# Optimization experiments

Hardware: AMD Instinct MI355X
Metric: run time of the kernel (lower is better)

## Reference

```python
import jax, jax.numpy as jnp
import numpy as np

EPS = 1e-6

def rmsnorm(x, w):
    v = jnp.mean(jnp.square(x), axis=-1, keepdims=True)
    return x * jax.lax.rsqrt(v + EPS) * w

def setup_inputs() -> dict:
    key = jax.random.key(0)
    ks = jax.random.split(key, 12)
    H, Di, L = 2048, 4096, 1024   # hidden, mamba inner (expand*H), seq tokens
    DT, N, K = 128, 16, 4         # dt_rank, d_state, d_conv
    F = 8192                      # MLP intermediate
    s = lambda k, shp, sc: jax.random.normal(k, shp, jnp.float32) * sc
    return dict(
        hidden_states=s(ks[0], (L, H), 1.0),
        in_ln_w=jnp.ones((H,), jnp.float32),
        pre_ff_ln_w=jnp.ones((H,), jnp.float32),
        in_proj_w=s(ks[1], (2 * Di, H), 0.02),
        conv_w=s(ks[2], (Di, K), 0.1),
        conv_b=s(ks[3], (Di,), 0.1),
        x_proj_w=s(ks[4], (DT + 2 * N, Di), 0.02),
        dt_ln_w=jnp.ones((DT,), jnp.float32),
        b_ln_w=jnp.ones((N,), jnp.float32),
        c_ln_w=jnp.ones((N,), jnp.float32),
        dt_proj_w=s(ks[5], (Di, DT), 0.02),
        dt_proj_b=s(ks[6], (Di,), 0.1),
        A=-jnp.exp(jax.random.uniform(ks[7], (Di, N), jnp.float32, -4.0, 0.0)),
        D=jnp.ones((Di,), jnp.float32),
        out_proj_w=s(ks[8], (H, Di), 0.02),
        gate_up_w=s(ks[9], (2 * F, H), 0.02),
        down_w=s(ks[10], (H, F), 0.02),
    )

def reference(hidden_states, in_ln_w, pre_ff_ln_w, in_proj_w, conv_w, conv_b,
              x_proj_w, dt_ln_w, b_ln_w, c_ln_w, dt_proj_w, dt_proj_b,
              A, D, out_proj_w, gate_up_w, down_w):
    residual = hidden_states
    x = rmsnorm(hidden_states, in_ln_w)
    # --- Mamba mixer (prefill / selective_scan path) ---
    proj = x @ in_proj_w.T                          # [L, 2*Di]
    Di = in_proj_w.shape[0] // 2
    h, gate = proj[:, :Di], proj[:, Di:]
    # causal depthwise conv1d, kernel K, left pad K-1, then silu
    K = conv_w.shape[1]
    L = h.shape[0]
    hp = jnp.pad(h, ((K - 1, 0), (0, 0)))           # [L+K-1, Di]
    idx = jnp.arange(L)[:, None] + jnp.arange(K)[None, :]
    h = jnp.einsum('lkd,dk->ld', hp[idx], conv_w) + conv_b
    h = jax.nn.silu(h)
    # ssm parameters
    ssm = h @ x_proj_w.T                            # [L, DT+2N]
    DTr = dt_ln_w.shape[0]
    N = b_ln_w.shape[0]
    dt = rmsnorm(ssm[:, :DTr], dt_ln_w)
    B = rmsnorm(ssm[:, DTr:DTr + N], b_ln_w)
    C = rmsnorm(ssm[:, DTr + N:], c_ln_w)
    delta = jax.nn.softplus(dt @ dt_proj_w.T + dt_proj_b)   # [L, Di]
    # selective scan (discretize then linear recurrence over L)
    dA = jnp.exp(delta[:, :, None] * A[None, :, :])         # [L, Di, N]
    dBu = delta[:, :, None] * B[:, None, :] * h[:, :, None] # [L, Di, N]
    def step(s, inp):
        da, dbu = inp
        s = da * s + dbu
        return s, s
    s0 = jnp.zeros((Di, N), jnp.float32)
    _, states = jax.lax.scan(step, s0, (dA, dBu))           # [L, Di, N]
    y = jnp.einsum('ldn,ln->ld', states, C) + h * D
    y = y * jax.nn.silu(gate)
    mixer_out = y @ out_proj_w.T                    # [L, H]
    # --- residual + pre-FF norm + gated MLP ---
    residual = residual + mixer_out
    x = rmsnorm(residual, pre_ff_ln_w)
    gu = x @ gate_up_w.T                            # [L, 2F]
    F = down_w.shape[1]
    x = jax.nn.silu(gu[:, :F]) * gu[:, F:]
    ff = x @ down_w.T
    return residual + ff
```

## Files before the change

kernel.cpp:

```cpp
#include <hip/hip_runtime.h>
#include <math.h>

typedef unsigned short u16;
typedef __bf16 bf16x8 __attribute__((ext_vector_type(8)));
typedef short s16x8 __attribute__((ext_vector_type(8)));
typedef short s16x4 __attribute__((ext_vector_type(4)));
typedef float f32x4 __attribute__((ext_vector_type(4)));

__device__ __forceinline__ u16 f2bf(float f) {
  union { float f; unsigned u; } v; v.f = f;
  unsigned u = v.u;
  unsigned r = u + 0x7fffu + ((u >> 16) & 1u);
  return (u16)(r >> 16);
}
__device__ __forceinline__ float bf2f(u16 h) {
  union { unsigned u; float f; } v; v.u = ((unsigned)h) << 16;
  return v.f;
}
__device__ __forceinline__ float fast_softplus(float x) {
  return (x > 20.f) ? x : __logf(1.f + __expf(x));
}
__device__ __forceinline__ float fast_sig(float x) {
  return __builtin_amdgcn_rcpf(1.f + __expf(-x));
}

__device__ __forceinline__ void gld_lds16(const u16* g, u16* l) {
  __builtin_amdgcn_global_load_lds(
      (const __attribute__((address_space(1))) unsigned int*)g,
      (__attribute__((address_space(3))) unsigned int*)l, 16, 0, 0);
}

__global__ __launch_bounds__(256)
void f32_to_bf16_k(const float* __restrict__ src, u16* __restrict__ dst,
                   int n, int n_valid) {
  int i = (blockIdx.x * 256 + threadIdx.x) * 4;
  if (i >= n) return;
  s16x4 o;
  if (i + 3 < n_valid) {
    float4 v = *(const float4*)(src + i);
    o[0] = (short)f2bf(v.x); o[1] = (short)f2bf(v.y);
    o[2] = (short)f2bf(v.z); o[3] = (short)f2bf(v.w);
  } else {
    o[0] = 0; o[1] = 0; o[2] = 0; o[3] = 0;
  }
  *(s16x4*)(dst + i) = o;
}

template <int BN, int MODE>
__global__ __launch_bounds__(256)
void gemm2(const u16* __restrict__ A, const u16* __restrict__ B,
           float* __restrict__ C, u16* __restrict__ Cb,
           const u16* __restrict__ aux, int M, int Nc, int K) {
  constexpr int NJ = BN / 32;
  constexpr int BISS = BN / 32;
  __shared__ __align__(16) u16 As[64 * 64];
  __shared__ __align__(16) u16 Bs[BN * 64];
  const int tid = threadIdx.x;
  const int tm0 = blockIdx.y * 64;
  const int tn0 = blockIdx.x * BN;
  const int wave = tid >> 6;
  const int lane = tid & 63;
  const int wm = (wave >> 1) * 32;
  const int wn = (wave & 1) * (BN / 2);
  const int frow = lane & 15;
  const int fc = lane >> 4;
  const int rmask = frow & 7;

  const int r0 = tid >> 3;
  const int csw = (((tid & 7) ^ (r0 & 7)) << 3);
  const u16* gA = A + (size_t)(tm0 + r0) * K + csw;
  const u16* gB = B + (size_t)(tn0 + r0) * K + csw;
  u16* lA = &As[tid * 8];
  u16* lB = &Bs[tid * 8];

  f32x4 acc[2][NJ];
  f32x4 zero = {0.f, 0.f, 0.f, 0.f};
#pragma unroll
  for (int i = 0; i < 2; ++i)
#pragma unroll
    for (int j = 0; j < NJ; ++j) acc[i][j] = zero;

  for (int kt = 0; kt < K; kt += 64) {
    __syncthreads();
    gld_lds16(gA, lA);
    gld_lds16(gA + (size_t)32 * K, lA + 2048);
#pragma unroll
    for (int b = 0; b < BISS; ++b)
      gld_lds16(gB + (size_t)32 * b * K, lB + b * 2048);
    gA += 64; gB += 64;
    __syncthreads();
#pragma unroll
    for (int s = 0; s < 2; ++s) {
      bf16x8 af[2], bfr[NJ];
#pragma unroll
      for (int i = 0; i < 2; ++i) {
        int addr = (wm + i * 16 + frow) * 64 + (((s * 4 + fc) ^ rmask) << 3);
        af[i] = __builtin_bit_cast(bf16x8, *(const s16x8*)&As[addr]);
      }
#pragma unroll
      for (int j = 0; j < NJ; ++j) {
        int addr = (wn + j * 16 + frow) * 64 + (((s * 4 + fc) ^ rmask) << 3);
        bfr[j] = __builtin_bit_cast(bf16x8, *(const s16x8*)&Bs[addr]);
      }
#pragma unroll
      for (int i = 0; i < 2; ++i)
#pragma unroll
        for (int j = 0; j < NJ; ++j)
          acc[i][j] = __builtin_amdgcn_mfma_f32_16x16x32_bf16(af[i], bfr[j], acc[i][j], 0, 0, 0);
    }
  }
  const int ccol = lane & 15;
  const int crow = (lane >> 4) * 4;
#pragma unroll
  for (int i = 0; i < 2; ++i) {
#pragma unroll
    for (int j = 0; j < NJ; ++j) {
      int gn = tn0 + wn + j * 16 + ccol;
      if (gn < Nc) {
        size_t base = (size_t)(tm0 + wm + i * 16 + crow) * Nc + gn;
#pragma unroll
        for (int r = 0; r < 4; ++r) {
          float c = acc[i][j][r];
          size_t idx = base + (size_t)r * Nc;
          if (MODE == 0) {
            C[idx] = c;
          } else if (MODE == 1) {
            Cb[idx] = f2bf(c * fast_sig(c));
          } else {
            Cb[idx] = f2bf(c * bf2f(aux[idx]));
          }
        }
      }
    }
  }
}

template <int MODE, int SPLITK>
__global__ __launch_bounds__(256)
void gemm128(const u16* __restrict__ A, const u16* __restrict__ B,
             float* __restrict__ C, u16* __restrict__ Cb,
             const u16* __restrict__ aux, int M, int Nc, int K) {
  __shared__ __align__(16) u16 As[128 * 64];
  __shared__ __align__(16) u16 Bs[128 * 64];
  const int tid = threadIdx.x;
  const int tm0 = blockIdx.y * 128;
  const int tn0 = blockIdx.x * 128;
  const int kslice = K / SPLITK;
  const int k0 = blockIdx.z * kslice;
  const int wave = tid >> 6;
  const int lane = tid & 63;
  const int wm = (wave >> 1) * 64;
  const int wn = (wave & 1) * 64;
  const int frow = lane & 15;
  const int fc = lane >> 4;
  const int rmask = frow & 7;

  const int r0 = tid >> 3;
  const int csw = (((tid & 7) ^ (r0 & 7)) << 3);
  const u16* gA = A + (size_t)(tm0 + r0) * K + k0 + csw;
  const u16* gB = B + (size_t)(tn0 + r0) * K + k0 + csw;
  u16* lA = &As[tid * 8];
  u16* lB = &Bs[tid * 8];

  f32x4 acc[4][4];
  f32x4 zero = {0.f, 0.f, 0.f, 0.f};
#pragma unroll
  for (int i = 0; i < 4; ++i)
#pragma unroll
    for (int j = 0; j < 4; ++j) acc[i][j] = zero;

  for (int kt = 0; kt < kslice; kt += 64) {
    __syncthreads();
#pragma unroll
    for (int b = 0; b < 4; ++b) {
      gld_lds16(gA + (size_t)(32 * b) * K, lA + b * 2048);
      gld_lds16(gB + (size_t)(32 * b) * K, lB + b * 2048);
    }
    gA += 64; gB += 64;
    __syncthreads();
#pragma unroll
    for (int s = 0; s < 2; ++s) {
      bf16x8 af[4], bfr[4];
#pragma unroll
      for (int i = 0; i < 4; ++i) {
        int addr = (wm + i * 16 + frow) * 64 + (((s * 4 + fc) ^ rmask) << 3);
        af[i] = __builtin_bit_cast(bf16x8, *(const s16x8*)&As[addr]);
      }
#pragma unroll
      for (int j = 0; j < 4; ++j) {
        int addr = (wn + j * 16 + frow) * 64 + (((s * 4 + fc) ^ rmask) << 3);
        bfr[j] = __builtin_bit_cast(bf16x8, *(const s16x8*)&Bs[addr]);
      }
#pragma unroll
      for (int i = 0; i < 4; ++i)
#pragma unroll
        for (int j = 0; j < 4; ++j)
          acc[i][j] = __builtin_amdgcn_mfma_f32_16x16x32_bf16(af[i], bfr[j], acc[i][j], 0, 0, 0);
    }
  }
  const int ccol = lane & 15;
  const int crow = (lane >> 4) * 4;
  float* Cp = C + (size_t)blockIdx.z * ((size_t)M * Nc);
#pragma unroll
  for (int i = 0; i < 4; ++i) {
#pragma unroll
    for (int j = 0; j < 4; ++j) {
      int gn = tn0 + wn + j * 16 + ccol;
      size_t base = (size_t)(tm0 + wm + i * 16 + crow) * Nc + gn;
#pragma unroll
      for (int r = 0; r < 4; ++r) {
        float c = acc[i][j][r];
        size_t idx = base + (size_t)r * Nc;
        if (MODE == 0) {
          Cp[idx] = c;
        } else if (MODE == 1) {
          Cb[idx] = f2bf(c * fast_sig(c));
        } else {
          Cb[idx] = f2bf(c * bf2f(aux[idx]));
        }
      }
    }
  }
}

__device__ inline float block_reduce_sum_256(float v) {
  __shared__ float red[4];
  int lane = threadIdx.x & 63, wave = threadIdx.x >> 6;
#pragma unroll
  for (int m = 32; m > 0; m >>= 1) v += __shfl_xor(v, m, 64);
  if (lane == 0) red[wave] = v;
  __syncthreads();
  return red[0] + red[1] + red[2] + red[3];
}

__global__ __launch_bounds__(256)
void rmsnorm2048_k(const float* __restrict__ x, const float* __restrict__ w,
                   u16* __restrict__ y) {
  const int C = 2048;
  const int row = blockIdx.x;
  const int t = threadIdx.x;
  const float4* xr = (const float4*)(x + (size_t)row * C);
  float4 v0 = xr[t];
  float4 v1 = xr[t + 256];
  float ss = v0.x * v0.x + v0.y * v0.y + v0.z * v0.z + v0.w * v0.w +
             v1.x * v1.x + v1.y * v1.y + v1.z * v1.z + v1.w * v1.w;
  float tot = block_reduce_sum_256(ss);
  float sc = rsqrtf(tot * (1.0f / C) + 1e-6f);
  const float4* wr = (const float4*)w;
  float4 w0 = wr[t], w1 = wr[t + 256];
  u16* yr = y + (size_t)row * C;
  s16x4 o0, o1;
  o0[0] = (short)f2bf(v0.x * sc * w0.x); o0[1] = (short)f2bf(v0.y * sc * w0.y);
  o0[2] = (short)f2bf(v0.z * sc * w0.z); o0[3] = (short)f2bf(v0.w * sc * w0.w);
  o1[0] = (short)f2bf(v1.x * sc * w1.x); o1[1] = (short)f2bf(v1.y * sc * w1.y);
  o1[2] = (short)f2bf(v1.z * sc * w1.z); o1[3] = (short)f2bf(v1.w * sc * w1.w);
  *(s16x4*)(yr + t * 4) = o0;
  *(s16x4*)(yr + 1024 + t * 4) = o1;
}

__global__ __launch_bounds__(256)
void add_rmsnorm4_k(const float* __restrict__ a, const float* __restrict__ p,
                    const float* __restrict__ w, float* __restrict__ resid,
                    u16* __restrict__ y) {
  const int C = 2048;
  const size_t S = (size_t)1024 * 2048;
  const int row = blockIdx.x;
  const int t = threadIdx.x;
  const float4* ar = (const float4*)(a + (size_t)row * C);
  float4 v0 = ar[t], v1 = ar[t + 256];
#pragma unroll
  for (int s = 0; s < 4; ++s) {
    const float4* br = (const float4*)(p + s * S + (size_t)row * C);
    float4 u0 = br[t], u1 = br[t + 256];
    v0.x += u0.x; v0.y += u0.y; v0.z += u0.z; v0.w += u0.w;
    v1.x += u1.x; v1.y += u1.y; v1.z += u1.z; v1.w += u1.w;
  }
  float4* rr = (float4*)(resid + (size_t)row * C);
  rr[t] = v0; rr[t + 256] = v1;
  float ss = v0.x * v0.x + v0.y * v0.y + v0.z * v0.z + v0.w * v0.w +
             v1.x * v1.x + v1.y * v1.y + v1.z * v1.z + v1.w * v1.w;
  float tot = block_reduce_sum_256(ss);
  float sc = rsqrtf(tot * (1.0f / C) + 1e-6f);
  const float4* wr = (const float4*)w;
  float4 w0 = wr[t], w1 = wr[t + 256];
  u16* yr = y + (size_t)row * C;
  s16x4 o0, o1;
  o0[0] = (short)f2bf(v0.x * sc * w0.x); o0[1] = (short)f2bf(v0.y * sc * w0.y);
  o0[2] = (short)f2bf(v0.z * sc * w0.z); o0[3] = (short)f2bf(v0.w * sc * w0.w);
  o1[0] = (short)f2bf(v1.x * sc * w1.x); o1[1] = (short)f2bf(v1.y * sc * w1.y);
  o1[2] = (short)f2bf(v1.z * sc * w1.z); o1[3] = (short)f2bf(v1.w * sc * w1.w);
  *(s16x4*)(yr + t * 4) = o0;
  *(s16x4*)(yr + 1024 + t * 4) = o1;
}

__global__ __launch_bounds__(256)
void conv_silu_k(const float* __restrict__ proj, const float* __restrict__ cw,
                 const float* __restrict__ cb, u16* __restrict__ h) {
  const int Di = 4096, LD = 8192;
  int idx = blockIdx.x * 256 + threadIdx.x;
  int d = idx & (Di - 1);
  int l = idx >> 12;
  float4 w = *(const float4*)(cw + (size_t)d * 4);
  float acc = cb[d];
  int ls0 = l - 3;
  if (ls0 >= 0) acc += proj[(size_t)ls0 * LD + d] * w.x;
  if (ls0 + 1 >= 0) acc += proj[(size_t)(ls0 + 1) * LD + d] * w.y;
  if (ls0 + 2 >= 0) acc += proj[(size_t)(ls0 + 2) * LD + d] * w.z;
  acc += proj[(size_t)l * LD + d] * w.w;
  h[idx] = f2bf(acc * fast_sig(acc));
}

__global__ __launch_bounds__(64)
void ssm_norm_k(const float* __restrict__ ssm, const float* __restrict__ dtw,
                const float* __restrict__ bw, const float* __restrict__ cw,
                u16* __restrict__ dtn, float* __restrict__ Bn,
                float* __restrict__ Cn) {
  int l = blockIdx.x;
  int lane = threadIdx.x;
  const float* r = ssm + (size_t)l * 160;
  float d0 = r[lane];
  float d1 = r[lane + 64];
  float bv = (lane < 16) ? r[128 + lane] : 0.f;
  float cv = (lane < 16) ? r[144 + lane] : 0.f;
  float sd = d0 * d0 + d1 * d1;
  float sb = bv * bv;
  float sc = cv * cv;
#pragma unroll
  for (int m = 32; m > 0; m >>= 1) {
    sd += __shfl_xor(sd, m, 64);
    sb += __shfl_xor(sb, m, 64);
    sc += __shfl_xor(sc, m, 64);
  }
  float scd = rsqrtf(sd * (1.f / 128.f) + 1e-6f);
  float scb = rsqrtf(sb * (1.f / 16.f) + 1e-6f);
  float scc = rsqrtf(sc * (1.f / 16.f) + 1e-6f);
  dtn[(size_t)l * 128 + lane] = f2bf(d0 * scd * dtw[lane]);
  dtn[(size_t)l * 128 + lane + 64] = f2bf(d1 * scd * dtw[lane + 64]);
  if (lane < 16) {
    Bn[(size_t)l * 16 + lane] = bv * scb * bw[lane];
    Cn[(size_t)l * 16 + lane] = cv * scc * cw[lane];
  }
}

#define NCH 32
#define CHL 32

__global__ __launch_bounds__(256)
void scan_p1(const float* __restrict__ dpre, const float* __restrict__ dtb,
             const u16* __restrict__ h, const float* __restrict__ Bn,
             const float* __restrict__ Amat,
             float* __restrict__ carryA, float* __restrict__ carryS) {
  const int Di = 4096;
  int chunk = blockIdx.x & (NCH - 1);
  int d = (blockIdx.x >> 5) * 256 + threadIdx.x;
  __shared__ float Bs[CHL * 16];
  for (int i = threadIdx.x; i < CHL * 16; i += 256)
    Bs[i] = Bn[(size_t)chunk * CHL * 16 + i];
  __syncthreads();
  float a[16];
#pragma unroll
  for (int q = 0; q < 4; ++q)
    *(float4*)&a[q * 4] = *(const float4*)(Amat + (size_t)d * 16 + q * 4);
  float bias = dtb[d];
  float s[16];
#pragma unroll
  for (int n = 0; n < 16; ++n) s[n] = 0.f;
  float sumdel = 0.f;
  int l0 = chunk * CHL;
#pragma unroll 4
  for (int j = 0; j < CHL; ++j) {
    int l = l0 + j;
    float del = fast_softplus(dpre[(size_t)l * Di + d] + bias);
    float hv = bf2f(h[(size_t)l * Di + d]);
    sumdel += del;
    float c = del * hv;
#pragma unroll
    for (int n = 0; n < 16; ++n) {
      float dA = __expf(del * a[n]);
      s[n] = dA * s[n] + c * Bs[j * 16 + n];
    }
  }
  size_t base = (size_t)chunk * 65536 + (size_t)d * 16;
#pragma unroll
  for (int n = 0; n < 16; ++n) {
    carryA[base + n] = __expf(sumdel * a[n]);
    carryS[base + n] = s[n];
  }
}

__global__ __launch_bounds__(256)
void scan_p2(const float* __restrict__ carryA, float* __restrict__ carryS) {
  int p = blockIdx.x * 256 + threadIdx.x;
  float cin = 0.f;
#pragma unroll
  for (int c = 0; c < NCH; ++c) {
    float av = carryA[(size_t)c * 65536 + p];
    float sv = carryS[(size_t)c * 65536 + p];
    float nx = av * cin + sv;
    carryS[(size_t)c * 65536 + p] = cin;
    cin = nx;
  }
}

__global__ __launch_bounds__(256)
void scan_p3(const float* __restrict__ dpre, const float* __restrict__ dtb,
             const u16* __restrict__ h, const float* __restrict__ Bn,
             const float* __restrict__ Cn, const float* __restrict__ Amat,
             const float* __restrict__ Dw, const float* __restrict__ proj,
             const float* __restrict__ carryS, u16* __restrict__ y) {
  const int Di = 4096;
  int chunk = blockIdx.x & (NCH - 1);
  int d = (blockIdx.x >> 5) * 256 + threadIdx.x;
  __shared__ float Bs[CHL * 16];
  __shared__ float Cs[CHL * 16];
  for (int i = threadIdx.x; i < CHL * 16; i += 256) {
    Bs[i] = Bn[(size_t)chunk * CHL * 16 + i];
    Cs[i] = Cn[(size_t)chunk * CHL * 16 + i];
  }
  __syncthreads();
  float a[16];
#pragma unroll
  for (int q = 0; q < 4; ++q)
    *(float4*)&a[q * 4] = *(const float4*)(Amat + (size_t)d * 16 + q * 4);
  float bias = dtb[d];
  float Dd = Dw[d];
  float s[16];
  size_t base = (size_t)chunk * 65536 + (size_t)d * 16;
#pragma unroll
  for (int q = 0; q < 4; ++q)
    *(float4*)&s[q * 4] = *(const float4*)(carryS + base + q * 4);
  int l0 = chunk * CHL;
#pragma unroll 2
  for (int j = 0; j < CHL; ++j) {
    int l = l0 + j;
    float del = fast_softplus(dpre[(size_t)l * Di + d] + bias);
    float hv = bf2f(h[(size_t)l * Di + d]);
    float c = del * hv;
    float p = 0.f;
#pragma unroll
    for (int n = 0; n < 16; ++n) {
      float dA = __expf(del * a[n]);
      s[n] = dA * s[n] + c * Bs[j * 16 + n];
      p += s[n] * Cs[j * 16 + n];
    }
    float g = proj[(size_t)l * 8192 + 4096 + d];
    float yv = p + hv * Dd;
    y[(size_t)l * Di + d] = f2bf(yv * g * fast_sig(g));
  }
}

__global__ __launch_bounds__(256)
void add4_k(float* __restrict__ out, const float* __restrict__ p) {
  const size_t S = (size_t)1024 * 2048;
  int i = blockIdx.x * 256 + threadIdx.x;
  float4 a = ((const float4*)out)[i];
#pragma unroll
  for (int s = 0; s < 4; ++s) {
    float4 b = ((const float4*)(p + s * S))[i];
    a.x += b.x; a.y += b.y; a.z += b.z; a.w += b.w;
  }
  ((float4*)out)[i] = a;
}

extern "C" void kernel_launch(void* const* d_in, const int* in_sizes, int n_in,
                              void* d_out, int out_size, void* d_ws, size_t ws_size,
                              hipStream_t stream) {
  const float* hidden      = (const float*)d_in[0];
  const float* in_ln_w     = (const float*)d_in[1];
  const float* pre_ff_ln_w = (const float*)d_in[2];
  const float* in_proj_w   = (const float*)d_in[3];
  const float* conv_w      = (const float*)d_in[4];
  const float* conv_b      = (const float*)d_in[5];
  const float* x_proj_w    = (const float*)d_in[6];
  const float* dt_ln_w     = (const float*)d_in[7];
  const float* b_ln_w      = (const float*)d_in[8];
  const float* c_ln_w      = (const float*)d_in[9];
  const float* dt_proj_w   = (const float*)d_in[10];
  const float* dt_proj_b   = (const float*)d_in[11];
  const float* Amat        = (const float*)d_in[12];
  const float* Dw          = (const float*)d_in[13];
  const float* out_proj_w  = (const float*)d_in[14];
  const float* gate_up_w   = (const float*)d_in[15];
  const float* down_w      = (const float*)d_in[16];
  float* out = (float*)d_out;
  float* ws = (float*)d_ws;

  const int L = 1024, H = 2048, Di = 4096, F = 8192;

  u16*   wbuf   = (u16*)ws;
  float* carryA = ws + 2097152;
  float* carryS = ws + 4194304;
  float* proj   = ws + 8388608;
  float* dpre   = ws + 16777216;
  u16*   hbuf   = (u16*)(ws + 20971520);
  u16*   xnorm  = (u16*)(ws + 23068672);
  float* ssm    = ws + 24117248;
  u16*   dtn    = (u16*)(ws + 24281088);
  float* Bn     = ws + 24346624;
  float* Cn     = ws + 24363008;
  u16*   ybuf   = (u16*)(ws + 24379392);
  float* mixp   = ws + 8388608;
  u16*   x2     = (u16*)(ws + 18874368);
  u16*   sg     = (u16*)(ws + 8388608);
  u16*   x3     = (u16*)(ws + 12582912);
  float* ffp    = ws + 16777216;

  rmsnorm2048_k<<<L, 256, 0, stream>>>(hidden, in_ln_w, xnorm);
  f32_to_bf16_k<<<16384, 256, 0, stream>>>(in_proj_w, wbuf, 16777216, 16777216);
  gemm128<0, 1><<<dim3(64, 8), 256, 0, stream>>>(xnorm, wbuf, proj, nullptr, nullptr, L, 8192, 2048);
  conv_silu_k<<<(L * Di) / 256, 256, 0, stream>>>(proj, conv_w, conv_b, hbuf);
  f32_to_bf16_k<<<1024, 256, 0, stream>>>(x_proj_w, wbuf, 1048576, 655360);
  gemm2<64, 0><<<dim3(4, 16), 256, 0, stream>>>(hbuf, wbuf, ssm, nullptr, nullptr, L, 160, 4096);
  ssm_norm_k<<<L, 64, 0, stream>>>(ssm, dt_ln_w, b_ln_w, c_ln_w, dtn, Bn, Cn);
  f32_to_bf16_k<<<512, 256, 0, stream>>>(dt_proj_w, wbuf, 524288, 524288);
  gemm2<128, 0><<<dim3(32, 16), 256, 0, stream>>>(dtn, wbuf, dpre, nullptr, nullptr, L, 4096, 128);
  scan_p1<<<16 * NCH, 256, 0, stream>>>(dpre, dt_proj_b, hbuf, Bn, Amat, carryA, carryS);
  scan_p2<<<256, 256, 0, stream>>>(carryA, carryS);
  scan_p3<<<16 * NCH, 256, 0, stream>>>(dpre, dt_proj_b, hbuf, Bn, Cn, Amat, Dw, proj, carryS, ybuf);
  f32_to_bf16_k<<<8192, 256, 0, stream>>>(out_proj_w, wbuf, 8388608, 8388608);
  gemm128<0, 4><<<dim3(16, 8, 4), 256, 0, stream>>>(ybuf, wbuf, mixp, nullptr, nullptr, L, 2048, 4096);
  add_rmsnorm4_k<<<L, 256, 0, stream>>>(hidden, mixp, pre_ff_ln_w, out, x2);
  f32_to_bf16_k<<<16384, 256, 0, stream>>>(gate_up_w, wbuf, 16777216, 16777216);
  gemm128<1, 1><<<dim3(64, 8), 256, 0, stream>>>(x2, wbuf, nullptr, sg, nullptr, L, 8192, 2048);
  f32_to_bf16_k<<<16384, 256, 0, stream>>>(gate_up_w + 16777216, wbuf, 16777216, 16777216);
  gemm128<2, 1><<<dim3(64, 8), 256, 0, stream>>>(x2, wbuf, nullptr, x3, sg, L, 8192, 2048);
  f32_to_bf16_k<<<16384, 256, 0, stream>>>(down_w, wbuf, 16777216, 16777216);
  gemm128<0, 4><<<dim3(16, 8, 4), 256, 0, stream>>>(x3, wbuf, ffp, nullptr, nullptr, L, 2048, 8192);
  add4_k<<<(L * H / 4) / 256, 256, 0, stream>>>(out, ffp);
}
```

Before: 685.2 us.

## Double-buffer gemm128 LDS tiles and split-K the x_proj GEMM

gemm128 now keeps two LDS buffers and issues the global-to-LDS loads for the next K tile before computing on the current one, with one barrier per iteration. This is meant to hide global load latency behind MFMA work. The small x_proj GEMM (160 output columns, K=4096), which launched only 64 blocks, is split four ways along K. ssm_norm_k sums the four partial results, raising parallelism for that GEMM. The cost is doubled LDS per block, which may lower occupancy, plus extra partial-sum traffic.

```diff
diff --git a/kernel.cpp b/kernel.cpp
--- a/kernel.cpp
+++ b/kernel.cpp
@@ -46,7 +46,7 @@
   *(s16x4*)(dst + i) = o;
 }
 
-template <int BN, int MODE>
+template <int BN, int MODE, int SPLITK>
 __global__ __launch_bounds__(256)
 void gemm2(const u16* __restrict__ A, const u16* __restrict__ B,
            float* __restrict__ C, u16* __restrict__ Cb,
@@ -58,6 +58,8 @@
   const int tid = threadIdx.x;
   const int tm0 = blockIdx.y * 64;
   const int tn0 = blockIdx.x * BN;
+  const int kslice = K / SPLITK;
+  const int k0 = blockIdx.z * kslice;
   const int wave = tid >> 6;
   const int lane = tid & 63;
   const int wm = (wave >> 1) * 32;
@@ -68,8 +70,8 @@
 
   const int r0 = tid >> 3;
   const int csw = (((tid & 7) ^ (r0 & 7)) << 3);
-  const u16* gA = A + (size_t)(tm0 + r0) * K + csw;
-  const u16* gB = B + (size_t)(tn0 + r0) * K + csw;
+  const u16* gA = A + (size_t)(tm0 + r0) * K + k0 + csw;
+  const u16* gB = B + (size_t)(tn0 + r0) * K + k0 + csw;
   u16* lA = &As[tid * 8];
   u16* lB = &Bs[tid * 8];
 
@@ -80,7 +82,7 @@
 #pragma unroll
     for (int j = 0; j < NJ; ++j) acc[i][j] = zero;
 
-  for (int kt = 0; kt < K; kt += 64) {
+  for (int kt = 0; kt < kslice; kt += 64) {
     __syncthreads();
     gld_lds16(gA, lA);
     gld_lds16(gA + (size_t)32 * K, lA + 2048);
@@ -111,6 +113,7 @@
   }
   const int ccol = lane & 15;
   const int crow = (lane >> 4) * 4;
+  float* Cp = C + (size_t)blockIdx.z * ((size_t)M * Nc);
 #pragma unroll
   for (int i = 0; i < 2; ++i) {
 #pragma unroll
@@ -123,7 +126,7 @@
           float c = acc[i][j][r];
           size_t idx = base + (size_t)r * Nc;
           if (MODE == 0) {
-            C[idx] = c;
+            Cp[idx] = c;
           } else if (MODE == 1) {
             Cb[idx] = f2bf(c * fast_sig(c));
           } else {
@@ -140,8 +143,8 @@
 void gemm128(const u16* __restrict__ A, const u16* __restrict__ B,
              float* __restrict__ C, u16* __restrict__ Cb,
              const u16* __restrict__ aux, int M, int Nc, int K) {
-  __shared__ __align__(16) u16 As[128 * 64];
-  __shared__ __align__(16) u16 Bs[128 * 64];
+  __shared__ __align__(16) u16 As[2 * 128 * 64];
+  __shared__ __align__(16) u16 Bs[2 * 128 * 64];
   const int tid = threadIdx.x;
   const int tm0 = blockIdx.y * 128;
   const int tn0 = blockIdx.x * 128;
@@ -169,26 +172,39 @@
 #pragma unroll
     for (int j = 0; j < 4; ++j) acc[i][j] = zero;
 
-  for (int kt = 0; kt < kslice; kt += 64) {
-    __syncthreads();
-#pragma unroll
-    for (int b = 0; b < 4; ++b) {
-      gld_lds16(gA + (size_t)(32 * b) * K, lA + b * 2048);
-      gld_lds16(gB + (size_t)(32 * b) * K, lB + b * 2048);
-    }
-    gA += 64; gB += 64;
-    __syncthreads();
+#pragma unroll
+  for (int b = 0; b < 4; ++b) {
+    gld_lds16(gA + (size_t)(32 * b) * K, lA + b * 2048);
+    gld_lds16(gB + (size_t)(32 * b) * K, lB + b * 2048);
+  }
+  gA += 64; gB += 64;
+  __syncthreads();
+
+  const int nt = kslice >> 6;
+  int buf = 0;
+  for (int kt = 0; kt < nt; ++kt) {
+    const int nb = buf ^ 1;
+    if (kt + 1 < nt) {
+#pragma unroll
+      for (int b = 0; b < 4; ++b) {
+        gld_lds16(gA + (size_t)(32 * b) * K, lA + nb * 8192 + b * 2048);
+        gld_lds16(gB + (size_t)(32 * b) * K, lB + nb * 8192 + b * 2048);
+      }
+      gA += 64; gB += 64;
+    }
+    __builtin_amdgcn_sched_barrier(0);
+    const int boff = buf * 8192;
 #pragma unroll
     for (int s = 0; s < 2; ++s) {
       bf16x8 af[4], bfr[4];
 #pragma unroll
       for (int i = 0; i < 4; ++i) {
-        int addr = (wm + i * 16 + frow) * 64 + (((s * 4 + fc) ^ rmask) << 3);
+        int addr = boff + (wm + i * 16 + frow) * 64 + (((s * 4 + fc) ^ rmask) << 3);
         af[i] = __builtin_bit_cast(bf16x8, *(const s16x8*)&As[addr]);
       }
 #pragma unroll
       for (int j = 0; j < 4; ++j) {
-        int addr = (wn + j * 16 + frow) * 64 + (((s * 4 + fc) ^ rmask) << 3);
+        int addr = boff + (wn + j * 16 + frow) * 64 + (((s * 4 + fc) ^ rmask) << 3);
         bfr[j] = __builtin_bit_cast(bf16x8, *(const s16x8*)&Bs[addr]);
       }
 #pragma unroll
@@ -197,7 +213,10 @@
         for (int j = 0; j < 4; ++j)
           acc[i][j] = __builtin_amdgcn_mfma_f32_16x16x32_bf16(af[i], bfr[j], acc[i][j], 0, 0, 0);
     }
-  }
+    __syncthreads();
+    buf = nb;
+  }
+
   const int ccol = lane & 15;
   const int crow = (lane >> 4) * 4;
   float* Cp = C + (size_t)blockIdx.z * ((size_t)M * Nc);
@@ -311,17 +330,24 @@
 }
 
 __global__ __launch_bounds__(64)
-void ssm_norm_k(const float* __restrict__ ssm, const float* __restrict__ dtw,
+void ssm_norm_k(const float* __restrict__ ssmp, const float* __restrict__ dtw,
                 const float* __restrict__ bw, const float* __restrict__ cw,
                 u16* __restrict__ dtn, float* __restrict__ Bn,
                 float* __restrict__ Cn) {
+  const size_t S = (size_t)1024 * 160;
   int l = blockIdx.x;
   int lane = threadIdx.x;
-  const float* r = ssm + (size_t)l * 160;
-  float d0 = r[lane];
-  float d1 = r[lane + 64];
-  float bv = (lane < 16) ? r[128 + lane] : 0.f;
-  float cv = (lane < 16) ? r[144 + lane] : 0.f;
+  float d0 = 0.f, d1 = 0.f, bv = 0.f, cv = 0.f;
+#pragma unroll
+  for (int s = 0; s < 4; ++s) {
+    const float* r = ssmp + s * S + (size_t)l * 160;
+    d0 += r[lane];
+    d1 += r[lane + 64];
+    if (lane < 16) {
+      bv += r[128 + lane];
+      cv += r[144 + lane];
+    }
+  }
   float sd = d0 * d0 + d1 * d1;
   float sb = bv * bv;
   float sc = cv * cv;
@@ -492,9 +518,9 @@
   float* carryS = ws + 4194304;
   float* proj   = ws + 8388608;
   float* dpre   = ws + 16777216;
+  float* ssmp   = ws + 16777216;
   u16*   hbuf   = (u16*)(ws + 20971520);
   u16*   xnorm  = (u16*)(ws + 23068672);
-  float* ssm    = ws + 24117248;
   u16*   dtn    = (u16*)(ws + 24281088);
   float* Bn     = ws + 24346624;
   float* Cn     = ws + 24363008;
@@ -510,10 +536,10 @@
   gemm128<0, 1><<<dim3(64, 8), 256, 0, stream>>>(xnorm, wbuf, proj, nullptr, nullptr, L, 8192, 2048);
   conv_silu_k<<<(L * Di) / 256, 256, 0, stream>>>(proj, conv_w, conv_b, hbuf);
   f32_to_bf16_k<<<1024, 256, 0, stream>>>(x_proj_w, wbuf, 1048576, 655360);
-  gemm2<64, 0><<<dim3(4, 16), 256, 0, stream>>>(hbuf, wbuf, ssm, nullptr, nullptr, L, 160, 4096);
-  ssm_norm_k<<<L, 64, 0, stream>>>(ssm, dt_ln_w, b_ln_w, c_ln_w, dtn, Bn, Cn);
+  gemm2<64, 0, 4><<<dim3(4, 16, 4), 256, 0, stream>>>(hbuf, wbuf, ssmp, nullptr, nullptr, L, 160, 4096);
+  ssm_norm_k<<<L, 64, 0, stream>>>(ssmp, dt_ln_w, b_ln_w, c_ln_w, dtn, Bn, Cn);
   f32_to_bf16_k<<<512, 256, 0, stream>>>(dt_proj_w, wbuf, 524288, 524288);
-  gemm2<128, 0><<<dim3(32, 16), 256, 0, stream>>>(dtn, wbuf, dpre, nullptr, nullptr, L, 4096, 128);
+  gemm2<128, 0, 1><<<dim3(32, 16), 256, 0, stream>>>(dtn, wbuf, dpre, nullptr, nullptr, L, 4096, 128);
   scan_p1<<<16 * NCH, 256, 0, stream>>>(dpre, dt_proj_b, hbuf, Bn, Amat, carryA, carryS);
   scan_p2<<<256, 256, 0, stream>>>(carryA, carryS);
   scan_p3<<<16 * NCH, 256, 0, stream>>>(dpre, dt_proj_b, hbuf, Bn, Cn, Amat, Dw, proj, carryS, ybuf);
```

After: 632.0 us. 7.8% less time.
